# Kernel tuning notes

Hardware: AMD Instinct MI355X
Metric: run time of the kernel (lower is better)

The kernel has to match this reference:

```python
import jax, jax.numpy as jnp
import numpy as np

VOCAB, D, H, L = 32000, 1024, 1024, 2
S, B = 512, 32
PAD = 1  # onmt.Constants.PAD -> embedding row zeroed


def setup_inputs() -> dict:
    key = jax.random.key(0)
    ks = jax.random.split(key, 12)
    sc = 0.05
    tokens = jax.random.randint(ks[0], (S, B), 0, VOCAB)
    h0 = jax.random.normal(ks[1], (L, B, H), jnp.float32)
    c0 = jax.random.normal(ks[2], (L, B, H), jnp.float32)
    emb = (jax.random.normal(ks[3], (VOCAB, D), jnp.float32) * sc).at[PAD].set(0.0)
    W_ih_0 = jax.random.normal(ks[4], (4 * H, D), jnp.float32) * sc
    W_hh_0 = jax.random.normal(ks[5], (4 * H, H), jnp.float32) * sc
    b_ih_0 = jax.random.normal(ks[6], (4 * H,), jnp.float32) * sc
    b_hh_0 = jax.random.normal(ks[7], (4 * H,), jnp.float32) * sc
    W_ih_1 = jax.random.normal(ks[8], (4 * H, H), jnp.float32) * sc
    W_hh_1 = jax.random.normal(ks[9], (4 * H, H), jnp.float32) * sc
    b_ih_1 = jax.random.normal(ks[10], (4 * H,), jnp.float32) * sc
    b_hh_1 = jax.random.normal(ks[11], (4 * H,), jnp.float32) * sc
    return dict(tokens=tokens, h0=h0, c0=c0, emb=emb,
                W_ih_0=W_ih_0, W_hh_0=W_hh_0, b_ih_0=b_ih_0, b_hh_0=b_hh_0,
                W_ih_1=W_ih_1, W_hh_1=W_hh_1, b_ih_1=b_ih_1, b_hh_1=b_hh_1)


def _lstm_cell(x, h, c, W_ih, W_hh, b_ih, b_hh):
    # PyTorch LSTMCell: gates = x W_ih^T + b_ih + h W_hh^T + b_hh ; order i,f,g,o
    gates = x @ W_ih.T + b_ih + h @ W_hh.T + b_hh  # [B, 4H]
    i, f, g, o = jnp.split(gates, 4, axis=-1)
    i = jax.nn.sigmoid(i); f = jax.nn.sigmoid(f)
    g = jnp.tanh(g); o = jax.nn.sigmoid(o)
    c_new = f * c + i * g
    h_new = o * jnp.tanh(c_new)
    return h_new, c_new


def reference(tokens, h0, c0, emb,
              W_ih_0, W_hh_0, b_ih_0, b_hh_0,
              W_ih_1, W_hh_1, b_ih_1, b_hh_1):
    x = emb[tokens]  # [S, B, D] embedding lookup
    layer_params = ((W_ih_0, W_hh_0, b_ih_0, b_hh_0),
                    (W_ih_1, W_hh_1, b_ih_1, b_hh_1))

    def step(carry, x_t):
        h, c = carry  # each [L, B, H]
        inp = x_t
        hs, cs = [], []
        for l in range(L):  # fixed small layer loop (structurally distinct params)
            h_l, c_l = _lstm_cell(inp, h[l], c[l], *layer_params[l])
            inp = h_l  # dropout=0.0 -> identity between layers and on output
            hs.append(h_l); cs.append(c_l)
        return (jnp.stack(hs), jnp.stack(cs)), inp

    (hF, cF), outputs = jax.lax.scan(step, (h0, c0), x)
    return outputs, (hF, cF)  # outputs: [S, B, H]
```

## Files before the change

kernel.cpp:

```cpp
#include <hip/hip_runtime.h>


typedef __bf16 bf16x8 __attribute__((ext_vector_type(8)));
typedef unsigned short u16x8 __attribute__((ext_vector_type(8)));
typedef float f32x4 __attribute__((ext_vector_type(4)));
typedef unsigned int u32x4 __attribute__((ext_vector_type(4)));

#define NSTEPS 512
#define TEAM   128
#define OUT_ELEMS 16777216
#define BH 32768

#define LDS_BYTES 151168
#define OFF_SC   131072
#define OFF_BIAS 149504
#define OFF_CST  149632
#define OFF_HST  150656

__device__ __forceinline__ unsigned short f2b(float f) {
    unsigned int u = __float_as_uint(f);
    u += 0x7fffu + ((u >> 16) & 1u);
    return (unsigned short)(u >> 16);
}
__device__ __forceinline__ float sigm(float x) { return 1.0f / (1.0f + __expf(-x)); }

__device__ __forceinline__ bf16x8 cvt8(const float* p) {
    float4 a = *(const float4*)p;
    float4 b = *(const float4*)(p + 4);
    bf16x8 r;
    r[0] = (__bf16)a.x; r[1] = (__bf16)a.y; r[2] = (__bf16)a.z; r[3] = (__bf16)a.w;
    r[4] = (__bf16)b.x; r[5] = (__bf16)b.y; r[6] = (__bf16)b.z; r[7] = (__bf16)b.w;
    return r;
}

__device__ __forceinline__ bf16x8 ld_mall16(const unsigned short* p) {
    u32x4 r;
    asm volatile("global_load_dwordx4 %0, %1, off sc0 sc1" : "=v"(r) : "v"(p));
    return __builtin_bit_cast(bf16x8, r);
}
__device__ __forceinline__ void st_mall16(unsigned short* p, u32x4 v) {
    asm volatile("global_store_dwordx4 %0, %1, off sc0 sc1" :: "v"(p), "v"(v) : "memory");
}
__device__ __forceinline__ void st_mall2(unsigned short* p, unsigned int v) {
    asm volatile("global_store_short %0, %1, off sc0 sc1" :: "v"(p), "v"(v) : "memory");
}
__device__ __forceinline__ void wait_vm0() {
    asm volatile("s_waitcnt vmcnt(0)" ::: "memory");
}
__device__ __forceinline__ void wait_vm16() {
    asm volatile("s_waitcnt vmcnt(16)" ::: "memory");
}
__device__ __forceinline__ unsigned int flag_ld(const unsigned int* p) {
    return __hip_atomic_load(p, __ATOMIC_RELAXED, __HIP_MEMORY_SCOPE_AGENT);
}
__device__ __forceinline__ void flag_st(unsigned int* p, unsigned int v) {
    __hip_atomic_store(p, v, __ATOMIC_RELAXED, __HIP_MEMORY_SCOPE_AGENT);
}
__device__ __forceinline__ void poll2(const unsigned int* f, int lane, unsigned int tgt) {
    while (flag_ld(f + lane) < tgt) __builtin_amdgcn_s_sleep(1);
    while (flag_ld(f + 64 + lane) < tgt) __builtin_amdgcn_s_sleep(1);
}

extern "C" __global__ __launch_bounds__(256, 1)
void lstm_persist(const int* __restrict__ tokens,
                  const float* __restrict__ h0in,
                  const float* __restrict__ c0in,
                  const float* __restrict__ emb,
                  const float* __restrict__ Wih0,
                  const float* __restrict__ Whh0,
                  const float* __restrict__ bih0,
                  const float* __restrict__ bhh0,
                  const float* __restrict__ Wih1,
                  const float* __restrict__ Whh1,
                  const float* __restrict__ bih1,
                  const float* __restrict__ bhh1,
                  float* __restrict__ dout,
                  unsigned short* __restrict__ h0b,
                  unsigned short* __restrict__ h1b,
                  unsigned int* __restrict__ cnt,
                  int R)
{
    extern __shared__ char smem[];
    unsigned short* wfrag = (unsigned short*)smem;
    float* sc   = (float*)(smem + OFF_SC);
    float* bias = (float*)(smem + OFF_BIAS);
    float* cst  = (float*)(smem + OFF_CST);
    unsigned short* hst = (unsigned short*)(smem + OFF_HST);

    const int tid  = threadIdx.x;
    const int w    = tid >> 6;
    const int lane = tid & 63;
    const int lm   = lane & 15;
    const int lq   = lane >> 4;
    const int blk  = blockIdx.x;
    const bool tB  = (blk >= TEAM);
    const int bid  = tB ? blk - TEAM : blk;
    const int n0   = bid * 8;

    const float* Wih = tB ? Wih1 : Wih0;
    const float* Whh = tB ? Whh1 : Whh0;
    const float* bi  = tB ? bih1 : bih0;
    const float* bh  = tB ? bhh1 : bhh0;
    unsigned int* flagA = cnt;
    unsigned int* flagB = cnt + TEAM;
    unsigned int* myflag = (tB ? flagB : flagA) + bid;

    {
        int u = tid & 7, b = tid >> 3;
        int loff = tB ? BH : 0;
        unsigned short v = f2b(h0in[loff + b * 1024 + n0 + u]);
        st_mall2((tB ? h1b : h0b) + (size_t)(R - 1) * BH + b * 1024 + n0 + u, (unsigned int)v);
    }

    for (int t = tid; t < 8192; t += 256) {
        int chunk = t >> 6; int l = t & 63;
        int mat = chunk >> 6; int rem = chunk & 63;
        int nt = rem >> 5; int ks = rem & 31;
        int n = l & 15, q = l >> 4;
        int cl = nt * 16 + n;
        int grow = (cl >> 3) * 1024 + n0 + (cl & 7);
        const float* src = (mat ? Whh : Wih) + (size_t)grow * 1024 + ks * 32 + q * 8;
        *(bf16x8*)(wfrag + chunk * 512 + l * 8) = cvt8(src);
    }
    if (tid < 32) {
        int grow = (tid >> 3) * 1024 + n0 + (tid & 7);
        bias[tid] = bi[grow] + bh[grow];
    }
    {
        int u = tid & 7, b = tid >> 3;
        int loff = tB ? BH : 0;
        cst[b * 8 + u] = c0in[loff + b * 1024 + n0 + u];
    }
    wait_vm0();
    __syncthreads();
    if (tid == 0) flag_st(myflag, 1u);

    f32x4 acc[2][2];
    bf16x8 pre[2][8];
    bf16x8 sa[2][8];
    const f32x4 zero = {0.f, 0.f, 0.f, 0.f};

    for (int s = 0; s < NSTEPS; ++s) {
        const int slotPrev = (s + R - 1) % R;
        const int slotCur  = s % R;
        const unsigned short* hs;
        int preMat, strMat;

        if (!tB) {
            #pragma unroll
            for (int mt = 0; mt < 2; ++mt) {
                const float* rowp = emb + (size_t)tokens[s * 32 + mt * 16 + lm] * 1024 + lq * 8;
                #pragma unroll
                for (int i = 0; i < 8; ++i)
                    pre[mt][i] = cvt8(rowp + (w * 8 + i) * 32);
            }
            if (w == 0)                   poll2(flagA, lane, (unsigned int)(s + 1));
            else if (w == 1 && s >= R)    poll2(flagB, lane, (unsigned int)(s - R + 2));
            __syncthreads();
            hs = h0b + (size_t)slotPrev * BH;  preMat = 0; strMat = 1;
        } else {
            if (w == 0)      poll2(flagB, lane, (unsigned int)(s + 1));
            else if (w == 1) poll2(flagA, lane, (unsigned int)(s + 2));
            __syncthreads();
            const unsigned short* h1src = h1b + (size_t)slotPrev * BH;
            #pragma unroll
            for (int mt = 0; mt < 2; ++mt)
                #pragma unroll
                for (int i = 0; i < 8; ++i)
                    pre[mt][i] = ld_mall16(h1src + (mt * 16 + lm) * 1024 + (w * 8 + i) * 32 + lq * 8);
            hs = h0b + (size_t)slotCur * BH;  preMat = 1; strMat = 0;
        }

        #pragma unroll
        for (int mt = 0; mt < 2; ++mt)
            #pragma unroll
            for (int i = 0; i < 8; ++i)
                sa[mt][i] = ld_mall16(hs + (mt * 16 + lm) * 1024 + (w * 8 + i) * 32 + lq * 8);

        acc[0][0] = zero; acc[0][1] = zero; acc[1][0] = zero; acc[1][1] = zero;

        if (tB) { wait_vm16(); __builtin_amdgcn_sched_barrier(0); }

        #pragma unroll
        for (int i = 0; i < 8; ++i) {
            int ks = w * 8 + i;
            bf16x8 bp0 = *(const bf16x8*)(wfrag + ((preMat * 2 + 0) * 32 + ks) * 512 + lane * 8);
            bf16x8 bp1 = *(const bf16x8*)(wfrag + ((preMat * 2 + 1) * 32 + ks) * 512 + lane * 8);
            acc[0][0] = __builtin_amdgcn_mfma_f32_16x16x32_bf16(pre[0][i], bp0, acc[0][0], 0, 0, 0);
            acc[0][1] = __builtin_amdgcn_mfma_f32_16x16x32_bf16(pre[0][i], bp1, acc[0][1], 0, 0, 0);
            acc[1][0] = __builtin_amdgcn_mfma_f32_16x16x32_bf16(pre[1][i], bp0, acc[1][0], 0, 0, 0);
            acc[1][1] = __builtin_amdgcn_mfma_f32_16x16x32_bf16(pre[1][i], bp1, acc[1][1], 0, 0, 0);
        }

        wait_vm0();
        __builtin_amdgcn_sched_barrier(0);

        #pragma unroll
        for (int i = 0; i < 8; ++i) {
            int ks = w * 8 + i;
            bf16x8 bs0 = *(const bf16x8*)(wfrag + ((strMat * 2 + 0) * 32 + ks) * 512 + lane * 8);
            bf16x8 bs1 = *(const bf16x8*)(wfrag + ((strMat * 2 + 1) * 32 + ks) * 512 + lane * 8);
            acc[0][0] = __builtin_amdgcn_mfma_f32_16x16x32_bf16(sa[0][i], bs0, acc[0][0], 0, 0, 0);
            acc[0][1] = __builtin_amdgcn_mfma_f32_16x16x32_bf16(sa[0][i], bs1, acc[0][1], 0, 0, 0);
            acc[1][0] = __builtin_amdgcn_mfma_f32_16x16x32_bf16(sa[1][i], bs0, acc[1][0], 0, 0, 0);
            acc[1][1] = __builtin_amdgcn_mfma_f32_16x16x32_bf16(sa[1][i], bs1, acc[1][1], 0, 0, 0);
        }

        #pragma unroll
        for (int mt = 0; mt < 2; ++mt) {
            #pragma unroll
            for (int nt = 0; nt < 2; ++nt) {
                f32x4 a = acc[mt][nt];
                int col = nt * 16 + lm;
                int rb = w * 32 + mt * 16 + lq * 4;
                sc[(rb + 0) * 36 + col] = a[0];
                sc[(rb + 1) * 36 + col] = a[1];
                sc[(rb + 2) * 36 + col] = a[2];
                sc[(rb + 3) * 36 + col] = a[3];
            }
        }
        __syncthreads();

        {
            int u = tid & 7, b = tid >> 3;
            float G[4];
            #pragma unroll
            for (int g = 0; g < 4; ++g) {
                int col = g * 8 + u;
                float v = bias[col];
                #pragma unroll
                for (int w2 = 0; w2 < 4; ++w2) v += sc[(w2 * 32 + b) * 36 + col];
                G[g] = v;
            }
            float ig = sigm(G[0]);
            float fg = sigm(G[1]);
            float gg = tanhf(G[2]);
            float og = sigm(G[3]);
            float cOld = cst[b * 8 + u];
            float cNew = fg * cOld + ig * gg;
            float hNew = og * tanhf(cNew);
            cst[b * 8 + u] = cNew;
            hst[b * 8 + u] = f2b(hNew);
            __syncthreads();

            if (tid < 32) {
                u32x4 v16 = *(const u32x4*)(hst + tid * 8);
                unsigned short* dst = (tB ? h1b : h0b) + (size_t)slotCur * BH + tid * 1024 + n0;
                st_mall16(dst, v16);
            }
            if (w == 0) {
                wait_vm0();
                if (tid == 0) flag_st(myflag, (unsigned int)(s + 2));
            }

            int off = b * 1024 + n0 + u;
            if (tB) {
                dout[(size_t)s * BH + off] = hNew;
                if (s == NSTEPS - 1) {
                    dout[OUT_ELEMS + BH + off] = hNew;
                    dout[OUT_ELEMS + 3 * BH + off] = cNew;
                }
            } else if (s == NSTEPS - 1) {
                dout[OUT_ELEMS + off] = hNew;
                dout[OUT_ELEMS + 2 * BH + off] = cNew;
            }
        }
    }
}

extern "C" void kernel_launch(void* const* d_in, const int* in_sizes, int n_in,
                              void* d_out, int out_size, void* d_ws, size_t ws_size,
                              hipStream_t stream) {
    hipFuncSetAttribute((const void*)lstm_persist,
                        hipFuncAttributeMaxDynamicSharedMemorySize, LDS_BYTES);
    hipMemsetAsync(d_ws, 0, 4096, stream);

    const int* tokens = (const int*)d_in[0];
    const float* h0   = (const float*)d_in[1];
    const float* c0   = (const float*)d_in[2];
    const float* emb  = (const float*)d_in[3];
    const float* Wih0 = (const float*)d_in[4];
    const float* Whh0 = (const float*)d_in[5];
    const float* bih0 = (const float*)d_in[6];
    const float* bhh0 = (const float*)d_in[7];
    const float* Wih1 = (const float*)d_in[8];
    const float* Whh1 = (const float*)d_in[9];
    const float* bih1 = (const float*)d_in[10];
    const float* bhh1 = (const float*)d_in[11];

    long long avail = (long long)ws_size - 4096;
    long long r = avail / (2LL * BH * 2);
    int R = (int)(r > NSTEPS ? NSTEPS : r);
    if (R < 2) R = 2;

    unsigned int* cnt = (unsigned int*)d_ws;
    unsigned short* h0b = (unsigned short*)((char*)d_ws + 4096);
    unsigned short* h1b = h0b + (size_t)R * BH;

    lstm_persist<<<dim3(256), dim3(256), LDS_BYTES, stream>>>(
        tokens, h0, c0, emb, Wih0, Whh0, bih0, bhh0, Wih1, Whh1, bih1, bhh1,
        (float*)d_out, h0b, h1b, cnt, R);
}
```

Before: 4.605 ms.

## Give each wave an independent output tile with per-wave flags, removing block barriers

The work split changes from splitting K across the four waves (followed by an LDS reduction and block-wide barriers) to giving each wave its own batch-half by unit-group tile over the full K. Each wave now runs the gate math for its own tile, keeps c in a register, and signals its own flag. Consumers poll four times as many flags, so the __syncthreads per timestep go away and waves synchronise independently. The cost is four times as many MFMAs per wave on a single accumulator chain, more global h loads per wave, a bounded poll loop that gives up after a limit, and a larger flag array.

```diff
diff --git a/kernel.cpp b/kernel.cpp
--- a/kernel.cpp
+++ b/kernel.cpp
@@ -2,7 +2,6 @@
 
 
 typedef __bf16 bf16x8 __attribute__((ext_vector_type(8)));
-typedef unsigned short u16x8 __attribute__((ext_vector_type(8)));
 typedef float f32x4 __attribute__((ext_vector_type(4)));
 typedef unsigned int u32x4 __attribute__((ext_vector_type(4)));
 
@@ -10,12 +9,10 @@
 #define TEAM   128
 #define OUT_ELEMS 16777216
 #define BH 32768
-
-#define LDS_BYTES 151168
+#define POLL_LIMIT (1u << 22)
+
+#define LDS_BYTES 135424
 #define OFF_SC   131072
-#define OFF_BIAS 149504
-#define OFF_CST  149632
-#define OFF_HST  150656
 
 __device__ __forceinline__ unsigned short f2b(float f) {
     unsigned int u = __float_as_uint(f);
@@ -33,33 +30,40 @@
     return r;
 }
 
-__device__ __forceinline__ bf16x8 ld_mall16(const unsigned short* p) {
+__device__ __forceinline__ bf16x8 ld16(const unsigned short* p) {
     u32x4 r;
     asm volatile("global_load_dwordx4 %0, %1, off sc0 sc1" : "=v"(r) : "v"(p));
     return __builtin_bit_cast(bf16x8, r);
 }
-__device__ __forceinline__ void st_mall16(unsigned short* p, u32x4 v) {
-    asm volatile("global_store_dwordx4 %0, %1, off sc0 sc1" :: "v"(p), "v"(v) : "memory");
-}
-__device__ __forceinline__ void st_mall2(unsigned short* p, unsigned int v) {
+__device__ __forceinline__ void st2_mall(unsigned short* p, unsigned int v) {
     asm volatile("global_store_short %0, %1, off sc0 sc1" :: "v"(p), "v"(v) : "memory");
 }
-__device__ __forceinline__ void wait_vm0() {
-    asm volatile("s_waitcnt vmcnt(0)" ::: "memory");
-}
-__device__ __forceinline__ void wait_vm16() {
-    asm volatile("s_waitcnt vmcnt(16)" ::: "memory");
-}
+#define WVC(N) do { asm volatile("s_waitcnt vmcnt(" #N ")" ::: "memory"); \
+                    __builtin_amdgcn_sched_barrier(0); } while (0)
+
 __device__ __forceinline__ unsigned int flag_ld(const unsigned int* p) {
     return __hip_atomic_load(p, __ATOMIC_RELAXED, __HIP_MEMORY_SCOPE_AGENT);
 }
 __device__ __forceinline__ void flag_st(unsigned int* p, unsigned int v) {
     __hip_atomic_store(p, v, __ATOMIC_RELAXED, __HIP_MEMORY_SCOPE_AGENT);
 }
-__device__ __forceinline__ void poll2(const unsigned int* f, int lane, unsigned int tgt) {
-    while (flag_ld(f + lane) < tgt) __builtin_amdgcn_s_sleep(1);
-    while (flag_ld(f + 64 + lane) < tgt) __builtin_amdgcn_s_sleep(1);
-}
+__device__ __forceinline__ void poll4(const unsigned int* f, int lane,
+                                      unsigned int tgt, int* alive) {
+    if (!*alive) return;
+    unsigned int it = 0;
+    for (;;) {
+        unsigned int a = flag_ld(f + lane);
+        unsigned int b = flag_ld(f + 64 + lane);
+        unsigned int c = flag_ld(f + 128 + lane);
+        unsigned int d = flag_ld(f + 192 + lane);
+        if (a >= tgt && b >= tgt && c >= tgt && d >= tgt) break;
+        if (++it > POLL_LIMIT) { *alive = 0; break; }
+        __builtin_amdgcn_s_sleep(1);
+    }
+    asm volatile("" ::: "memory");
+}
+
+#define MM(aop, ck) acc = __builtin_amdgcn_mfma_f32_16x16x32_bf16((aop), wfv[(ck) * 64 + lane], acc, 0, 0, 0)
 
 extern "C" __global__ __launch_bounds__(256, 1)
 void lstm_persist(const int* __restrict__ tokens,
@@ -82,188 +86,154 @@
 {
     extern __shared__ char smem[];
     unsigned short* wfrag = (unsigned short*)smem;
-    float* sc   = (float*)(smem + OFF_SC);
-    float* bias = (float*)(smem + OFF_BIAS);
-    float* cst  = (float*)(smem + OFF_CST);
-    unsigned short* hst = (unsigned short*)(smem + OFF_HST);
+    const bf16x8* wfv = (const bf16x8*)smem;
+    float* scAll = (float*)(smem + OFF_SC);
 
     const int tid  = threadIdx.x;
     const int w    = tid >> 6;
     const int lane = tid & 63;
     const int lm   = lane & 15;
     const int lq   = lane >> 4;
+    const int m    = w & 1;
+    const int n    = w >> 1;
     const int blk  = blockIdx.x;
     const bool tB  = (blk >= TEAM);
     const int bid  = tB ? blk - TEAM : blk;
     const int n0   = bid * 8;
-
-    const float* Wih = tB ? Wih1 : Wih0;
-    const float* Whh = tB ? Whh1 : Whh0;
-    const float* bi  = tB ? bih1 : bih0;
-    const float* bh  = tB ? bhh1 : bhh0;
-    unsigned int* flagA = cnt;
-    unsigned int* flagB = cnt + TEAM;
-    unsigned int* myflag = (tB ? flagB : flagA) + bid;
-
-    {
-        int u = tid & 7, b = tid >> 3;
-        int loff = tB ? BH : 0;
-        unsigned short v = f2b(h0in[loff + b * 1024 + n0 + u]);
-        st_mall2((tB ? h1b : h0b) + (size_t)(R - 1) * BH + b * 1024 + n0 + u, (unsigned int)v);
-    }
+    const int b16  = lane >> 2;
+    const int u    = lane & 3;
+
+    const float* preW = tB ? Whh1 : Wih0;
+    const float* strW = tB ? Wih1 : Whh0;
+    const float* bi   = tB ? bih1 : bih0;
+    const float* bh_  = tB ? bhh1 : bhh0;
+    unsigned int* flagT = cnt + (tB ? 512 : 0);
+    unsigned int* flagO = cnt + (tB ? 0 : 512);
+    unsigned int* myflag = flagT + m * 256 + n * 128 + bid;
+    const unsigned int* ownQ = flagT + m * 256;
+    const unsigned int* othQ = flagO + m * 256;
+    unsigned short* myring = tB ? h1b : h0b;
+
+    const int uoff   = n0 + n * 4 + u;
+    const int rowOff = (m * 16 + b16) * 1024 + uoff;
+    const int loff   = tB ? BH : 0;
+
+    st2_mall(myring + (size_t)(R - 1) * BH + rowOff, (unsigned int)f2b(h0in[loff + rowOff]));
+    float cReg  = c0in[loff + rowOff];
+    float bias0 = bi[0 * 1024 + uoff] + bh_[0 * 1024 + uoff];
+    float bias1 = bi[1 * 1024 + uoff] + bh_[1 * 1024 + uoff];
+    float bias2 = bi[2 * 1024 + uoff] + bh_[2 * 1024 + uoff];
+    float bias3 = bi[3 * 1024 + uoff] + bh_[3 * 1024 + uoff];
 
     for (int t = tid; t < 8192; t += 256) {
         int chunk = t >> 6; int l = t & 63;
-        int mat = chunk >> 6; int rem = chunk & 63;
-        int nt = rem >> 5; int ks = rem & 31;
-        int n = l & 15, q = l >> 4;
-        int cl = nt * 16 + n;
-        int grow = (cl >> 3) * 1024 + n0 + (cl & 7);
-        const float* src = (mat ? Whh : Wih) + (size_t)grow * 1024 + ks * 32 + q * 8;
-        *(bf16x8*)(wfrag + chunk * 512 + l * 8) = cvt8(src);
+        int cn = chunk >> 6; int ks = chunk & 63;
+        int lmc = l & 15, lq2 = l >> 4;
+        int g = lmc >> 2, uu = lmc & 3;
+        int grow = g * 1024 + n0 + cn * 4 + uu;
+        const float* W = (ks < 32) ? preW : strW;
+        *(bf16x8*)(wfrag + chunk * 512 + l * 8) = cvt8(W + (size_t)grow * 1024 + (ks & 31) * 32 + lq2 * 8);
     }
-    if (tid < 32) {
-        int grow = (tid >> 3) * 1024 + n0 + (tid & 7);
-        bias[tid] = bi[grow] + bh[grow];
-    }
-    {
-        int u = tid & 7, b = tid >> 3;
-        int loff = tB ? BH : 0;
-        cst[b * 8 + u] = c0in[loff + b * 1024 + n0 + u];
-    }
-    wait_vm0();
+    asm volatile("s_waitcnt vmcnt(0)" ::: "memory");
     __syncthreads();
-    if (tid == 0) flag_st(myflag, 1u);
-
-    f32x4 acc[2][2];
-    bf16x8 pre[2][8];
-    bf16x8 sa[2][8];
+    if (lane == 0) flag_st(myflag, 1u);
+
+    float* scw = scAll + w * 272;
+    const int sidx = lane * 4 + lq * 4;
+    const int radd = lq * 4 + (b16 & 3);
+
+    int alive = 1;
+    f32x4 acc;
     const f32x4 zero = {0.f, 0.f, 0.f, 0.f};
 
     for (int s = 0; s < NSTEPS; ++s) {
         const int slotPrev = (s + R - 1) % R;
         const int slotCur  = s % R;
-        const unsigned short* hs;
-        int preMat, strMat;
+        acc = zero;
 
         if (!tB) {
-            #pragma unroll
-            for (int mt = 0; mt < 2; ++mt) {
-                const float* rowp = emb + (size_t)tokens[s * 32 + mt * 16 + lm] * 1024 + lq * 8;
+            const int tok = tokens[s * 32 + m * 16 + lm];
+            const float* er = emb + (size_t)tok * 1024 + lq * 8;
+            #pragma unroll
+            for (int gp = 0; gp < 4; ++gp) {
+                bf16x8 ef[8];
                 #pragma unroll
-                for (int i = 0; i < 8; ++i)
-                    pre[mt][i] = cvt8(rowp + (w * 8 + i) * 32);
+                for (int j = 0; j < 8; ++j) ef[j] = cvt8(er + (gp * 8 + j) * 32);
+                #pragma unroll
+                for (int j = 0; j < 8; ++j) MM(ef[j], n * 64 + gp * 8 + j);
             }
-            if (w == 0)                   poll2(flagA, lane, (unsigned int)(s + 1));
-            else if (w == 1 && s >= R)    poll2(flagB, lane, (unsigned int)(s - R + 2));
-            __syncthreads();
-            hs = h0b + (size_t)slotPrev * BH;  preMat = 0; strMat = 1;
+            poll4(ownQ, lane, (unsigned int)(s + 1), &alive);
+            if (s >= R) poll4(othQ, lane, (unsigned int)(s - R + 2), &alive);
+            const unsigned short* hr = h0b + (size_t)slotPrev * BH + (m * 16 + lm) * 1024 + lq * 8;
+            bf16x8 s0[16], s1[16];
+            #pragma unroll
+            for (int kk = 0; kk < 16; ++kk) s0[kk] = ld16(hr + kk * 32);
+            #pragma unroll
+            for (int kk = 0; kk < 16; ++kk) s1[kk] = ld16(hr + (16 + kk) * 32);
+            WVC(16);
+            #pragma unroll
+            for (int kk = 0; kk < 16; ++kk) MM(s0[kk], n * 64 + 32 + kk);
+            WVC(0);
+            #pragma unroll
+            for (int kk = 0; kk < 16; ++kk) MM(s1[kk], n * 64 + 48 + kk);
         } else {
-            if (w == 0)      poll2(flagB, lane, (unsigned int)(s + 1));
-            else if (w == 1) poll2(flagA, lane, (unsigned int)(s + 2));
-            __syncthreads();
-            const unsigned short* h1src = h1b + (size_t)slotPrev * BH;
-            #pragma unroll
-            for (int mt = 0; mt < 2; ++mt)
-                #pragma unroll
-                for (int i = 0; i < 8; ++i)
-                    pre[mt][i] = ld_mall16(h1src + (mt * 16 + lm) * 1024 + (w * 8 + i) * 32 + lq * 8);
-            hs = h0b + (size_t)slotCur * BH;  preMat = 1; strMat = 0;
+            poll4(ownQ, lane, (unsigned int)(s + 1), &alive);
+            const unsigned short* pr = h1b + (size_t)slotPrev * BH + (m * 16 + lm) * 1024 + lq * 8;
+            bf16x8 p0[16], p1[16];
+            #pragma unroll
+            for (int kk = 0; kk < 16; ++kk) p0[kk] = ld16(pr + kk * 32);
+            #pragma unroll
+            for (int kk = 0; kk < 16; ++kk) p1[kk] = ld16(pr + (16 + kk) * 32);
+            poll4(othQ, lane, (unsigned int)(s + 2), &alive);
+            const unsigned short* hr = h0b + (size_t)slotCur * BH + (m * 16 + lm) * 1024 + lq * 8;
+            WVC(16);
+            #pragma unroll
+            for (int kk = 0; kk < 16; ++kk) MM(p0[kk], n * 64 + kk);
+            bf16x8 s0[16];
+            #pragma unroll
+            for (int kk = 0; kk < 16; ++kk) s0[kk] = ld16(hr + kk * 32);
+            WVC(16);
+            #pragma unroll
+            for (int kk = 0; kk < 16; ++kk) MM(p1[kk], n * 64 + 16 + kk);
+            bf16x8 s1[16];
+            #pragma unroll
+            for (int kk = 0; kk < 16; ++kk) s1[kk] = ld16(hr + (16 + kk) * 32);
+            WVC(16);
+            #pragma unroll
+            for (int kk = 0; kk < 16; ++kk) MM(s0[kk], n * 64 + 32 + kk);
+            WVC(0);
+            #pragma unroll
+            for (int kk = 0; kk < 16; ++kk) MM(s1[kk], n * 64 + 48 + kk);
         }
 
-        #pragma unroll
-        for (int mt = 0; mt < 2; ++mt)
-            #pragma unroll
-            for (int i = 0; i < 8; ++i)
-                sa[mt][i] = ld_mall16(hs + (mt * 16 + lm) * 1024 + (w * 8 + i) * 32 + lq * 8);
-
-        acc[0][0] = zero; acc[0][1] = zero; acc[1][0] = zero; acc[1][1] = zero;
-
-        if (tB) { wait_vm16(); __builtin_amdgcn_sched_barrier(0); }
-
-        #pragma unroll
-        for (int i = 0; i < 8; ++i) {
-            int ks = w * 8 + i;
-            bf16x8 bp0 = *(const bf16x8*)(wfrag + ((preMat * 2 + 0) * 32 + ks) * 512 + lane * 8);
-            bf16x8 bp1 = *(const bf16x8*)(wfrag + ((preMat * 2 + 1) * 32 + ks) * 512 + lane * 8);
-            acc[0][0] = __builtin_amdgcn_mfma_f32_16x16x32_bf16(pre[0][i], bp0, acc[0][0], 0, 0, 0);
-            acc[0][1] = __builtin_amdgcn_mfma_f32_16x16x32_bf16(pre[0][i], bp1, acc[0][1], 0, 0, 0);
-            acc[1][0] = __builtin_amdgcn_mfma_f32_16x16x32_bf16(pre[1][i], bp0, acc[1][0], 0, 0, 0);
-            acc[1][1] = __builtin_amdgcn_mfma_f32_16x16x32_bf16(pre[1][i], bp1, acc[1][1], 0, 0, 0);
-        }
-
-        wait_vm0();
+        *(f32x4*)(scw + sidx) = acc;
+        asm volatile("s_waitcnt lgkmcnt(0)" ::: "memory");
         __builtin_amdgcn_sched_barrier(0);
-
-        #pragma unroll
-        for (int i = 0; i < 8; ++i) {
-            int ks = w * 8 + i;
-            bf16x8 bs0 = *(const bf16x8*)(wfrag + ((strMat * 2 + 0) * 32 + ks) * 512 + lane * 8);
-            bf16x8 bs1 = *(const bf16x8*)(wfrag + ((strMat * 2 + 1) * 32 + ks) * 512 + lane * 8);
-            acc[0][0] = __builtin_amdgcn_mfma_f32_16x16x32_bf16(sa[0][i], bs0, acc[0][0], 0, 0, 0);
-            acc[0][1] = __builtin_amdgcn_mfma_f32_16x16x32_bf16(sa[0][i], bs1, acc[0][1], 0, 0, 0);
-            acc[1][0] = __builtin_amdgcn_mfma_f32_16x16x32_bf16(sa[1][i], bs0, acc[1][0], 0, 0, 0);
-            acc[1][1] = __builtin_amdgcn_mfma_f32_16x16x32_bf16(sa[1][i], bs1, acc[1][1], 0, 0, 0);
-        }
-
-        #pragma unroll
-        for (int mt = 0; mt < 2; ++mt) {
-            #pragma unroll
-            for (int nt = 0; nt < 2; ++nt) {
-                f32x4 a = acc[mt][nt];
-                int col = nt * 16 + lm;
-                int rb = w * 32 + mt * 16 + lq * 4;
-                sc[(rb + 0) * 36 + col] = a[0];
-                sc[(rb + 1) * 36 + col] = a[1];
-                sc[(rb + 2) * 36 + col] = a[2];
-                sc[(rb + 3) * 36 + col] = a[3];
+        float G0 = scw[(lq * 16 + 0 + u) * 4 + radd] + bias0;
+        float G1 = scw[(lq * 16 + 4 + u) * 4 + radd] + bias1;
+        float G2 = scw[(lq * 16 + 8 + u) * 4 + radd] + bias2;
+        float G3 = scw[(lq * 16 + 12 + u) * 4 + radd] + bias3;
+        float ig = sigm(G0);
+        float fg = sigm(G1);
+        float gg = tanhf(G2);
+        float og = sigm(G3);
+        float cN = fg * cReg + ig * gg;
+        float hN = og * tanhf(cN);
+        cReg = cN;
+
+        st2_mall(myring + (size_t)slotCur * BH + rowOff, (unsigned int)f2b(hN));
+        WVC(0);
+        if (lane == 0) flag_st(myflag, (unsigned int)(s + 2));
+
+        if (tB) {
+            dout[(size_t)s * BH + rowOff] = hN;
+            if (s == NSTEPS - 1) {
+                dout[OUT_ELEMS + BH + rowOff] = hN;
+                dout[OUT_ELEMS + 3 * BH + rowOff] = cN;
             }
-        }
-        __syncthreads();
-
-        {
-            int u = tid & 7, b = tid >> 3;
-            float G[4];
-            #pragma unroll
-            for (int g = 0; g < 4; ++g) {
-                int col = g * 8 + u;
-                float v = bias[col];
-                #pragma unroll
-                for (int w2 = 0; w2 < 4; ++w2) v += sc[(w2 * 32 + b) * 36 + col];
-                G[g] = v;
-            }
-            float ig = sigm(G[0]);
-            float fg = sigm(G[1]);
-            float gg = tanhf(G[2]);
-            float og = sigm(G[3]);
-            float cOld = cst[b * 8 + u];
-            float cNew = fg * cOld + ig * gg;
-            float hNew = og * tanhf(cNew);
-            cst[b * 8 + u] = cNew;
-            hst[b * 8 + u] = f2b(hNew);
-            __syncthreads();
-
-            if (tid < 32) {
-                u32x4 v16 = *(const u32x4*)(hst + tid * 8);
-                unsigned short* dst = (tB ? h1b : h0b) + (size_t)slotCur * BH + tid * 1024 + n0;
-                st_mall16(dst, v16);
-            }
-            if (w == 0) {
-                wait_vm0();
-                if (tid == 0) flag_st(myflag, (unsigned int)(s + 2));
-            }
-
-            int off = b * 1024 + n0 + u;
-            if (tB) {
-                dout[(size_t)s * BH + off] = hNew;
-                if (s == NSTEPS - 1) {
-                    dout[OUT_ELEMS + BH + off] = hNew;
-                    dout[OUT_ELEMS + 3 * BH + off] = cNew;
-                }
-            } else if (s == NSTEPS - 1) {
-                dout[OUT_ELEMS + off] = hNew;
-                dout[OUT_ELEMS + 2 * BH + off] = cNew;
-            }
+        } else if (s == NSTEPS - 1) {
+            dout[OUT_ELEMS + rowOff] = hN;
+            dout[OUT_ELEMS + 2 * BH + rowOff] = cN;
         }
     }
 }
```

Result: slower. 8.899 ms (+93.3%).
